# Kernel optimization log

Hardware: AMD Instinct MI355X
Metric: run time of the kernel (lower is better)

Reference implementation:

```python
import jax, jax.numpy as jnp
import numpy as np

DN = ('NCHW', 'OIHW', 'NCHW')  # dimension numbers for all convs


def _dwconv(x, w, dim):
    # depthwise conv, valid padding; w: (dim,1,kh,kw)
    return jax.lax.conv_general_dilated(
        x, w, window_strides=(1, 1), padding='VALID',
        dimension_numbers=DN, feature_group_count=dim)


def setup_inputs() -> dict:
    key = jax.random.key(0)
    ks = jax.random.split(key, 5)
    B, C, H, W = 16, 256, 96, 96
    REP_K = 3
    x = jax.random.normal(ks[0], (B, C, H, W), dtype=jnp.float32)
    meta_pe = jax.random.normal(ks[1], (1, C, H, 1), dtype=jnp.float32) * 0.02
    weight = jax.random.normal(ks[2], (C, 1, H, 1), dtype=jnp.float32) * 0.02
    bias = jnp.zeros((C,), dtype=jnp.float32)
    rep_weight = jax.random.normal(ks[3], (C, 1, REP_K, 1), dtype=jnp.float32) * 0.02
    return {'x': x, 'meta_pe': meta_pe, 'weight': weight, 'bias': bias,
            'rep_weight': rep_weight}


def reference(x, meta_pe, weight, bias, rep_weight):
    # type == 'H': circular padding / conv along the H axis (kernels (K,1))
    dim = x.shape[1]
    rep_k = rep_weight.shape[2]
    # positional embedding add (broadcast over batch and W)
    x = x + meta_pe
    # local branch: circular pad by rep_k-1 rows, small depthwise conv
    x_cat = jnp.concatenate([x, x[:, :, :rep_k - 1, :]], axis=2)
    x_rep = _dwconv(x_cat, rep_weight, dim)
    # global branch: circular pad by H-1 rows, full-height depthwise conv + bias
    x_cat = jnp.concatenate([x, x[:, :, :-1, :]], axis=2)
    x_gcc = _dwconv(x_cat, weight, dim) + bias[None, :, None, None]
    return x_rep + x_gcc
```

## Files before the change

### kernel.cpp

```cpp
#include <hip/hip_runtime.h>

#define B_   16
#define C_   256
#define HH   96
#define WW   96
#define TPB  192

typedef _Float16 half8 __attribute__((ext_vector_type(8)));
typedef float   f32x16 __attribute__((ext_vector_type(16)));

__global__ __launch_bounds__(TPB) void fused_circ_conv_mfma(
    const float* __restrict__ x,
    const float* __restrict__ meta_pe,
    const float* __restrict__ weight,
    const float* __restrict__ bias,
    const float* __restrict__ rep_weight,
    float* __restrict__ out)
{
    __shared__ __align__(16) float sX[3][HH][32];
    __shared__ float sW[2 * HH];

    const int tid  = threadIdx.x;
    const int blk  = blockIdx.x;
    const int c    = blk & (C_ - 1);
    const size_t base = (size_t)blk * (HH * WW);

    const int lane = tid & 63;
    const int wv   = tid >> 6;
    const int r32  = lane & 31;
    const int g    = lane >> 5;

    {
        int k = (tid < HH) ? tid : (tid - HH);
        float w_ = weight[c * HH + k];
        if (k < 3) w_ += rep_weight[c * 3 + k];
        sW[tid] = w_;
    }

    {
        const int q  = lane & 7;
        const int jr = lane >> 3;
        const float* __restrict__ xg = x + base + wv * 32 + q * 4;
        const float* __restrict__ pe = meta_pe + c * HH;
        float* __restrict__ sxw = &sX[wv][0][0];
#pragma unroll
        for (int t = 0; t < 12; ++t) {
            const int j = t * 8 + jr;
            float4 v = *(const float4*)(xg + (size_t)j * WW);
            float m = pe[j];
            v.x += m; v.y += m; v.z += m; v.w += m;
            *(float4*)(sxw + j * 32 + q * 4) = v;
        }
    }
    __syncthreads();

    half8 ah[6], al[6];
#pragma unroll
    for (int s = 0; s < 6; ++s) {
        const float* wp = sW + (96 + s * 16 + g * 8 - r32);
#pragma unroll
        for (int e = 0; e < 8; ++e) {
            float w_ = wp[e];
            _Float16 h = (_Float16)w_;
            ah[s][e] = h;
            al[s][e] = (_Float16)(w_ - (float)h);
        }
    }

    half8 bh[6], bl[6];
    {
        const float* __restrict__ sxw = &sX[wv][0][0];
#pragma unroll
        for (int kt = 0; kt < 6; ++kt) {
#pragma unroll
            for (int e = 0; e < 8; ++e) {
                float v = sxw[(kt * 16 + g * 8 + e) * 32 + r32];
                _Float16 h = (_Float16)v;
                bh[kt][e] = h;
                bl[kt][e] = (_Float16)(v - (float)h);
            }
        }
    }

    const float bv = bias[c];
    float* __restrict__ op = out + base + (wv * 32 + r32);

#pragma unroll
    for (int m = 0; m < 3; ++m) {
        f32x16 acc;
#pragma unroll
        for (int i = 0; i < 16; ++i) acc[i] = 0.f;
#pragma unroll
        for (int kt = 0; kt < 6; ++kt) {
            const int s = (kt + 6 - 2 * m) % 6;
            acc = __builtin_amdgcn_mfma_f32_32x32x16_f16(ah[s], bh[kt], acc, 0, 0, 0);
            acc = __builtin_amdgcn_mfma_f32_32x32x16_f16(al[s], bh[kt], acc, 0, 0, 0);
            acc = __builtin_amdgcn_mfma_f32_32x32x16_f16(ah[s], bl[kt], acc, 0, 0, 0);
        }
#pragma unroll
        for (int reg = 0; reg < 16; ++reg) {
            int row = m * 32 + (reg & 3) + 8 * (reg >> 2) + 4 * g;
            op[(size_t)row * WW] = acc[reg] + bv;
        }
    }
}

extern "C" void kernel_launch(void* const* d_in, const int* in_sizes, int n_in,
                              void* d_out, int out_size, void* d_ws, size_t ws_size,
                              hipStream_t stream) {
    const float* x          = (const float*)d_in[0];
    const float* meta_pe    = (const float*)d_in[1];
    const float* weight     = (const float*)d_in[2];
    const float* bias       = (const float*)d_in[3];
    const float* rep_weight = (const float*)d_in[4];
    float* out = (float*)d_out;

    fused_circ_conv_mfma<<<dim3(B_ * C_), dim3(TPB), 0, stream>>>(
        x, meta_pe, weight, bias, rep_weight, out);
}
```

Baseline: 264.0 us.

## Split each (batch,channel) block into three single-wave blocks per W-slab

Each block previously held three waves, one per 32-column slab of W. Now each block is a single 64-thread wave that handles one slab, and the grid is three times larger. Blocks are smaller and more numerous, with less shared memory each, which may improve occupancy and scheduling granularity. In exchange, each of the three blocks reloads and preprocesses the same weight row, so that work is duplicated.

```diff
diff --git a/kernel.cpp b/kernel.cpp
--- a/kernel.cpp
+++ b/kernel.cpp
@@ -4,7 +4,7 @@
 #define C_   256
 #define HH   96
 #define WW   96
-#define TPB  192
+#define TPB  64
 
 typedef _Float16 half8 __attribute__((ext_vector_type(8)));
 typedef float   f32x16 __attribute__((ext_vector_type(16)));
@@ -17,73 +17,63 @@
     const float* __restrict__ rep_weight,
     float* __restrict__ out)
 {
-    __shared__ __align__(16) float sX[3][HH][32];
+    __shared__ __align__(16) float sX[HH][32];
     __shared__ float sW[2 * HH];
 
-    const int tid  = threadIdx.x;
+    const int lane = threadIdx.x;
     const int blk  = blockIdx.x;
-    const int c    = blk & (C_ - 1);
-    const size_t base = (size_t)blk * (HH * WW);
+    const int bc   = blk & (B_ * C_ - 1);
+    const int s    = blk >> 12;
+    const int c    = bc & (C_ - 1);
+    const size_t base = (size_t)bc * (HH * WW);
 
-    const int lane = tid & 63;
-    const int wv   = tid >> 6;
-    const int r32  = lane & 31;
-    const int g    = lane >> 5;
+    const int r32 = lane & 31;
+    const int g   = lane >> 5;
 
-    {
-        int k = (tid < HH) ? tid : (tid - HH);
+#pragma unroll
+    for (int t = 0; t < 3; ++t) {
+        int u = lane + TPB * t;
+        int k = (u < HH) ? u : u - HH;
         float w_ = weight[c * HH + k];
         if (k < 3) w_ += rep_weight[c * 3 + k];
-        sW[tid] = w_;
+        sW[u] = w_;
     }
 
     {
         const int q  = lane & 7;
         const int jr = lane >> 3;
-        const float* __restrict__ xg = x + base + wv * 32 + q * 4;
+        const float* __restrict__ xg = x + base + s * 32 + q * 4;
         const float* __restrict__ pe = meta_pe + c * HH;
-        float* __restrict__ sxw = &sX[wv][0][0];
 #pragma unroll
         for (int t = 0; t < 12; ++t) {
             const int j = t * 8 + jr;
             float4 v = *(const float4*)(xg + (size_t)j * WW);
             float m = pe[j];
             v.x += m; v.y += m; v.z += m; v.w += m;
-            *(float4*)(sxw + j * 32 + q * 4) = v;
+            *(float4*)(&sX[j][q * 4]) = v;
         }
     }
     __syncthreads();
 
-    half8 ah[6], al[6];
+    half8 ah[6], al[6], bh[6], bl[6];
 #pragma unroll
-    for (int s = 0; s < 6; ++s) {
-        const float* wp = sW + (96 + s * 16 + g * 8 - r32);
+    for (int t = 0; t < 6; ++t) {
+        const float* wp = sW + (96 + t * 16 + g * 8 - r32);
 #pragma unroll
         for (int e = 0; e < 8; ++e) {
             float w_ = wp[e];
             _Float16 h = (_Float16)w_;
-            ah[s][e] = h;
-            al[s][e] = (_Float16)(w_ - (float)h);
-        }
-    }
-
-    half8 bh[6], bl[6];
-    {
-        const float* __restrict__ sxw = &sX[wv][0][0];
-#pragma unroll
-        for (int kt = 0; kt < 6; ++kt) {
-#pragma unroll
-            for (int e = 0; e < 8; ++e) {
-                float v = sxw[(kt * 16 + g * 8 + e) * 32 + r32];
-                _Float16 h = (_Float16)v;
-                bh[kt][e] = h;
-                bl[kt][e] = (_Float16)(v - (float)h);
-            }
+            ah[t][e] = h;
+            al[t][e] = (_Float16)(w_ - (float)h);
+            float v = sX[t * 16 + g * 8 + e][r32];
+            _Float16 hb = (_Float16)v;
+            bh[t][e] = hb;
+            bl[t][e] = (_Float16)(v - (float)hb);
         }
     }
 
     const float bv = bias[c];
-    float* __restrict__ op = out + base + (wv * 32 + r32);
+    float* __restrict__ op = out + base + (s * 32 + r32);
 
 #pragma unroll
     for (int m = 0; m < 3; ++m) {
@@ -92,10 +82,10 @@
         for (int i = 0; i < 16; ++i) acc[i] = 0.f;
 #pragma unroll
         for (int kt = 0; kt < 6; ++kt) {
-            const int s = (kt + 6 - 2 * m) % 6;
-            acc = __builtin_amdgcn_mfma_f32_32x32x16_f16(ah[s], bh[kt], acc, 0, 0, 0);
-            acc = __builtin_amdgcn_mfma_f32_32x32x16_f16(al[s], bh[kt], acc, 0, 0, 0);
-            acc = __builtin_amdgcn_mfma_f32_32x32x16_f16(ah[s], bl[kt], acc, 0, 0, 0);
+            const int t = (kt + 6 - 2 * m) % 6;
+            acc = __builtin_amdgcn_mfma_f32_32x32x16_f16(ah[t], bh[kt], acc, 0, 0, 0);
+            acc = __builtin_amdgcn_mfma_f32_32x32x16_f16(al[t], bh[kt], acc, 0, 0, 0);
+            acc = __builtin_amdgcn_mfma_f32_32x32x16_f16(ah[t], bl[kt], acc, 0, 0, 0);
         }
 #pragma unroll
         for (int reg = 0; reg < 16; ++reg) {
@@ -115,6 +105,6 @@
     const float* rep_weight = (const float*)d_in[4];
     float* out = (float*)d_out;
 
-    fused_circ_conv_mfma<<<dim3(B_ * C_), dim3(TPB), 0, stream>>>(
+    fused_circ_conv_mfma<<<dim3(3 * B_ * C_), dim3(TPB), 0, stream>>>(
         x, meta_pe, weight, bias, rep_weight, out);
 }
```

Result: slower. 278.3 us (+5.4%).
